# Performance work log

Measured on AMD Instinct MI355X. Metric: run time of the kernel, lower is better.

Reference implementation:

```python
import jax, jax.numpy as jnp
import numpy as np

EPS = 1e-6
N_HEADS = 16
D_NOPE = 128   # qk_nope_head_dim == head_dim
D_ROPE = 64    # qk_rope_head_dim == head_dim // 2


def rmsnorm(x, g):
    # matches torch RMSNorm: normalize in fp32 then scale
    xf = x.astype(jnp.float32)
    n = xf * jax.lax.rsqrt(jnp.mean(xf * xf, axis=-1, keepdims=True) + EPS)
    return n.astype(x.dtype) * g


def rope(x):
    # x: [..., S, D]; rotary-embedding-torch convention: interleaved pairs, theta=10000
    S, D = x.shape[-2], x.shape[-1]
    freqs = 1.0 / (10000.0 ** (jnp.arange(0, D, 2, dtype=jnp.float32) / D))  # [D/2]
    ang = jnp.arange(S, dtype=jnp.float32)[:, None] * freqs                   # [S, D/2]
    ang = jnp.repeat(ang, 2, axis=-1)                                         # [S, D]
    cos, sin = jnp.cos(ang), jnp.sin(ang)
    x2 = x.reshape(*x.shape[:-1], D // 2, 2)
    xr = jnp.stack([-x2[..., 1], x2[..., 0]], axis=-1).reshape(x.shape)
    return x * cos + xr * sin


def setup_inputs() -> dict:
    key = jax.random.key(0)
    ks = jax.random.split(key, 9)
    def w(k, shape):
        return jax.random.normal(k, shape, dtype=jnp.float32) * (shape[0] ** -0.5)
    return {
        "x": jax.random.normal(ks[0], (2, 2048, 2048), dtype=jnp.float32),
        "w_dq": w(ks[1], (2048, 512)),
        "g_q": jnp.ones((512,), dtype=jnp.float32),
        "w_uq": w(ks[2], (512, 3072)),
        "w_dkv": w(ks[3], (2048, 512)),
        "g_kv": jnp.ones((512,), dtype=jnp.float32),
        "w_ukrope": w(ks[4], (2048, 64)),
        "w_uv": w(ks[5], (512, 2048)),
        "w_uknope": w(ks[6], (512, 2048)),
        "w_o": w(ks[7], (2048, 2048)),
    }


def reference(x, w_dq, g_q, w_uq, w_dkv, g_kv, w_ukrope, w_uv, w_uknope, w_o):
    B, S, _ = x.shape
    H, Dn, Dr = N_HEADS, D_NOPE, D_ROPE

    # low-rank KV path
    kv = rmsnorm(x @ w_dkv, g_kv)                                    # [B,S,512]
    k_nope = (kv @ w_uknope).reshape(B, S, H, Dn).transpose(0, 2, 1, 3)  # [B,H,S,Dn]
    v = (kv @ w_uv).reshape(B, S, H, Dn).transpose(0, 2, 1, 3)           # [B,H,S,Dn]
    k_rope = rope(x @ w_ukrope)                                      # [B,S,Dr] shared across heads

    # low-rank Q path
    q = rmsnorm(x @ w_dq, g_q) @ w_uq                                # [B,S,H*(Dn+Dr)]
    q = q.reshape(B, S, H, Dn + Dr).transpose(0, 2, 1, 3)            # [B,H,S,Dn+Dr]
    q_nope, q_rope = q[..., :Dn], rope(q[..., Dn:])

    # causal SDPA with head-shared rope keys folded into scores
    scale = 1.0 / jnp.sqrt(jnp.float32(Dn + Dr))
    scores = jnp.einsum("bhqd,bhkd->bhqk", q_nope, k_nope)
    scores = scores + jnp.einsum("bhqd,bkd->bhqk", q_rope, k_rope)
    scores = scores * scale
    causal = jnp.tril(jnp.ones((S, S), dtype=bool))
    scores = jnp.where(causal, scores, -jnp.inf)
    attn = jax.nn.softmax(scores, axis=-1)
    out = jnp.einsum("bhqk,bhkd->bhqd", attn, v)                     # [B,H,S,Dn]
    out = out.transpose(0, 2, 1, 3).reshape(B, S, H * Dn)
    return out @ w_o
```

## Files before the change

### kernel.cpp

```cpp
#include <hip/hip_runtime.h>
#include <hip/hip_bf16.h>


#define S_ 2048
#define H_ 16

typedef __bf16 bf16_t;
typedef __bf16 bf16x8 __attribute__((ext_vector_type(8)));
typedef __bf16 bf16x4_t __attribute__((ext_vector_type(4)));
typedef float f32x4 __attribute__((ext_vector_type(4)));

#define ASYNC_COPY16(gsrc, ldst)                                              \
  __builtin_amdgcn_global_load_lds(                                           \
      (const __attribute__((address_space(1))) void*)(gsrc),                  \
      (__attribute__((address_space(3))) void*)(ldst), 16, 0, 0)

#define QSCALE 0.1041177003f
#define FIXM 16.0f

struct TWDesc { const float* src; bf16_t* dst; int K, N, boff; };
struct TW7 { TWDesc d[7]; };

__global__ __launch_bounds__(256) void prep_all(const float* __restrict__ x,
                                                bf16_t* __restrict__ xb,
                                                float2* __restrict__ tab,
                                                TW7 t7) {
  __shared__ float t[32][33];
  int bid = blockIdx.x;
  int tid = threadIdx.x;
  if (bid < 8192) {
    int i = bid * 256 + tid;
    float4 v = ((const float4*)x)[i];
    bf16x4_t o = {(bf16_t)v.x, (bf16_t)v.y, (bf16_t)v.z, (bf16_t)v.w};
    ((bf16x4_t*)xb)[i] = o;
  } else if (bid < 8448) {
    int i = (bid - 8192) * 256 + tid;
    int j = i & 31, s = i >> 5;
    float freq = powf(10000.f, -(float)(2 * j) / 64.f);
    float ang = (float)s * freq;
    tab[i] = make_float2(cosf(ang), sinf(ang));
  } else {
    int e = 0;
#pragma unroll
    for (int i = 1; i < 7; i++)
      if (bid >= t7.d[i].boff) e = i;
    const float* src = t7.d[e].src;
    bf16_t* dst = t7.d[e].dst;
    int K = t7.d[e].K, N = t7.d[e].N;
    int lb = bid - t7.d[e].boff;
    int nx = N >> 5;
    int n0 = (lb % nx) * 32, k0 = (lb / nx) * 32;
    int tx = tid & 31, ty = tid >> 5;
#pragma unroll
    for (int i = 0; i < 4; i++)
      t[ty + i * 8][tx] = src[(size_t)(k0 + ty + i * 8) * N + n0 + tx];
    __syncthreads();
#pragma unroll
    for (int i = 0; i < 4; i++)
      dst[(size_t)(n0 + ty + i * 8) * K + k0 + tx] = (bf16_t)t[tx][ty + i * 8];
  }
}

template <typename OT, int MODE>
__global__ __launch_bounds__(256) void gemm_bt(const bf16_t* __restrict__ A,
                                               const bf16_t* __restrict__ Bt,
                                               OT* __restrict__ C, int M, int N,
                                               int K, int lda) {
  __shared__ bf16_t Asm[128 * 32];
  __shared__ bf16_t Bsm[128 * 32];
  int tid = threadIdx.x;
  int w = tid >> 6, lane = tid & 63;
  int lrow = lane & 15, lgrp = lane >> 4;
  int wr = w >> 1, wc = w & 1;
  int bm = blockIdx.y * 128, bn = blockIdx.x * 128;

  const bf16_t* Ab = A + (size_t)bm * lda;
  const bf16_t* Bb = Bt + (size_t)bn * K;

  int srow = (w << 5) + (lane >> 2);
  int schunk = lane & 3;

  int ra[4], rb[4];
#pragma unroll
  for (int m = 0; m < 4; m++) {
    int rowA = wr * 64 + m * 16 + lrow;
    ra[m] = rowA * 64 + ((lgrp * 16) ^ (((rowA >> 1) & 3) << 4));
    int rowB = wc * 64 + m * 16 + lrow;
    rb[m] = rowB * 64 + ((lgrp * 16) ^ (((rowB >> 1) & 3) << 4));
  }

  f32x4 acc[4][4] = {};

  for (int k0 = 0; k0 < K; k0 += 32) {
#pragma unroll
    for (int j = 0; j < 2; j++) {
      int row = srow + j * 16;
      int cs = schunk ^ ((row >> 1) & 3);
      ASYNC_COPY16(Ab + (size_t)row * lda + k0 + cs * 8,
                   (char*)Asm + (w << 11) + (j << 10));
      ASYNC_COPY16(Bb + (size_t)row * K + k0 + cs * 8,
                   (char*)Bsm + (w << 11) + (j << 10));
    }
    __syncthreads();
    bf16x8 af[4], bfr[4];
#pragma unroll
    for (int m = 0; m < 4; m++) {
      af[m] = *(const bf16x8*)((const char*)Asm + ra[m]);
      bfr[m] = *(const bf16x8*)((const char*)Bsm + rb[m]);
    }
#pragma unroll
    for (int m = 0; m < 4; m++)
#pragma unroll
      for (int n = 0; n < 4; n++)
        acc[m][n] =
            __builtin_amdgcn_mfma_f32_16x16x32_bf16(af[m], bfr[n], acc[m][n], 0, 0, 0);
    __syncthreads();
  }

#pragma unroll
  for (int m = 0; m < 4; m++)
#pragma unroll
    for (int n = 0; n < 4; n++)
#pragma unroll
      for (int j = 0; j < 4; j++) {
        int row = bm + wr * 64 + m * 16 + lgrp * 4 + j;
        int col = bn + wc * 64 + n * 16 + lrow;
        float val = acc[m][n][j];
        if (MODE == 0) {
          C[(size_t)row * N + col] = (OT)val;
        } else if (MODE == 6) {
          if (col < 1024) {
            ((bf16_t*)C)[(size_t)row * 1024 + col] = (bf16_t)val;
          } else if (col < 1088) {
            float* krf = (float*)((bf16_t*)C + (size_t)M * 1024);
            krf[(size_t)row * 64 + (col - 1024)] = val;
          }
        }
      }
}

__global__ __launch_bounds__(256) void gemm_qkv(const bf16_t* __restrict__ y,
                                                const bf16_t* __restrict__ uq_t,
                                                const bf16_t* __restrict__ ukn_t,
                                                bf16_t* __restrict__ Qp,
                                                bf16_t* __restrict__ Kp) {
  const int K = 512, lda = 1024, M = 4096;
  __shared__ bf16_t Asm[128 * 32];
  __shared__ bf16_t Bsm[128 * 32];
  int tid = threadIdx.x;
  int w = tid >> 6, lane = tid & 63;
  int lrow = lane & 15, lgrp = lane >> 4;
  int wr = w >> 1, wc = w & 1;
  int bnx = blockIdx.x;
  bool qpath = bnx < 24;
  const bf16_t* A = qpath ? y : (y + 512);
  const bf16_t* Bt = qpath ? uq_t : ukn_t;
  int bm = blockIdx.y * 128;
  int bn = (qpath ? bnx : bnx - 24) * 128;
  (void)M;

  const bf16_t* Ab = A + (size_t)bm * lda;
  const bf16_t* Bb = Bt + (size_t)bn * K;

  int srow = (w << 5) + (lane >> 2);
  int schunk = lane & 3;

  int ra[4], rb[4];
#pragma unroll
  for (int m = 0; m < 4; m++) {
    int rowA = wr * 64 + m * 16 + lrow;
    ra[m] = rowA * 64 + ((lgrp * 16) ^ (((rowA >> 1) & 3) << 4));
    int rowB = wc * 64 + m * 16 + lrow;
    rb[m] = rowB * 64 + ((lgrp * 16) ^ (((rowB >> 1) & 3) << 4));
  }

  f32x4 acc[4][4] = {};

  for (int k0 = 0; k0 < K; k0 += 32) {
#pragma unroll
    for (int j = 0; j < 2; j++) {
      int row = srow + j * 16;
      int cs = schunk ^ ((row >> 1) & 3);
      ASYNC_COPY16(Ab + (size_t)row * lda + k0 + cs * 8,
                   (char*)Asm + (w << 11) + (j << 10));
      ASYNC_COPY16(Bb + (size_t)row * K + k0 + cs * 8,
                   (char*)Bsm + (w << 11) + (j << 10));
    }
    __syncthreads();
    bf16x8 af[4], bfr[4];
#pragma unroll
    for (int m = 0; m < 4; m++) {
      af[m] = *(const bf16x8*)((const char*)Asm + ra[m]);
      bfr[m] = *(const bf16x8*)((const char*)Bsm + rb[m]);
    }
#pragma unroll
    for (int m = 0; m < 4; m++)
#pragma unroll
      for (int n = 0; n < 4; n++)
        acc[m][n] =
            __builtin_amdgcn_mfma_f32_16x16x32_bf16(af[m], bfr[n], acc[m][n], 0, 0, 0);
    __syncthreads();
  }

#pragma unroll
  for (int m = 0; m < 4; m++)
#pragma unroll
    for (int n = 0; n < 4; n++)
#pragma unroll
      for (int j = 0; j < 4; j++) {
        int row = bm + wr * 64 + m * 16 + lgrp * 4 + j;
        int col = bn + wc * 64 + n * 16 + lrow;
        float val = acc[m][n][j];
        int b = row >> 11, s = row & (S_ - 1);
        if (qpath) {
          unsigned h = (unsigned)col / 192u, f = (unsigned)col % 192u;
          Qp[((size_t)((b << 4) + h) * S_ + s) * 192 + f] = (bf16_t)(val * QSCALE);
        } else if (col < 2048) {
          int h = col >> 7, d = col & 127;
          Kp[((size_t)((b << 4) + h) * S_ + s) * 192 + d] = (bf16_t)val;
        } else {
          int c2 = col - 2048;
          int h = c2 >> 7, d = c2 & 127;
          bf16_t* VtP = Kp + (size_t)32 * S_ * 192;
          VtP[((size_t)((b << 4) + h) * 128 + d) * S_ + s] = (bf16_t)val;
        }
      }
}

__global__ __launch_bounds__(256) void rmsnorm_both(bf16_t* __restrict__ y,
                                                    const float* __restrict__ g_q,
                                                    const float* __restrict__ g_kv) {
  int bid = blockIdx.x;
  int row = bid >> 1, seg = bid & 1;
  const float* g = seg ? g_kv : g_q;
  bf16_t* p = y + (size_t)row * 1024 + seg * 512;
  int t = threadIdx.x;
  float v0 = (float)p[t], v1 = (float)p[t + 256];
  __shared__ float red[256];
  red[t] = v0 * v0 + v1 * v1;
  __syncthreads();
  for (int s = 128; s > 0; s >>= 1) {
    if (t < s) red[t] += red[t + s];
    __syncthreads();
  }
  float r = rsqrtf(red[0] / 512.f + 1e-6f);
  p[t] = (bf16_t)(v0 * r * g[t]);
  p[t + 256] = (bf16_t)(v1 * r * g[t + 256]);
}

__global__ __launch_bounds__(256) void rope_both(const float* __restrict__ krf,
                                                 const float2* __restrict__ tab,
                                                 bf16_t* __restrict__ Kp,
                                                 bf16_t* __restrict__ Qp) {
  int i = blockIdx.x * 256 + threadIdx.x;
  if (i < 4096 * 32) {
    int j = i & 31, row = i >> 5;
    int b = row >> 11, s = row & (S_ - 1);
    float v0 = krf[(size_t)row * 64 + 2 * j];
    float v1 = krf[(size_t)row * 64 + 2 * j + 1];
    float2 cs = tab[(s << 5) + j];
    bf16_t r0 = (bf16_t)(v0 * cs.x - v1 * cs.y);
    bf16_t r1 = (bf16_t)(v1 * cs.x + v0 * cs.y);
    union { bf16_t h[2]; unsigned u; } pk;
    pk.h[0] = r0; pk.h[1] = r1;
#pragma unroll
    for (int h = 0; h < 16; h++) {
      size_t base = ((size_t)((b << 4) + h) * S_ + s) * 192 + 128 + 2 * j;
      *(unsigned*)(Kp + base) = pk.u;
    }
  } else {
    int i2 = i - 4096 * 32;
    int j = i2 & 31;
    int s = (i2 >> 5) & (S_ - 1);
    int bh = i2 >> 16;
    float2 cs = tab[(s << 5) + j];
    size_t base = ((size_t)bh * S_ + s) * 192 + 128 + 2 * j;
    float x0 = (float)Qp[base], x1 = (float)Qp[base + 1];
    Qp[base] = (bf16_t)(x0 * cs.x - x1 * cs.y);
    Qp[base + 1] = (bf16_t)(x1 * cs.x + x0 * cs.y);
  }
}

__global__ __launch_bounds__(512) void flash_attn5(
    const bf16_t* __restrict__ Qp,
    const bf16_t* __restrict__ Kp,
    const bf16_t* __restrict__ Vt,
    bf16_t* __restrict__ o) {
  __shared__ alignas(16) char kls[2 * 64 * 384];
  __shared__ alignas(16) char vls[2 * 128 * 128];
  __shared__ alignas(16) bf16_t psh[8][16 * 64];

  int bid = blockIdx.x;
  int rest = bid >> 3;
  int p = rest & 7;
  int bh = (bid & 7) + ((rest >> 3) << 3);
  int b = bh >> 4;

  int tid = threadIdx.x;
  int w = tid >> 6;
  int lane = tid & 63;
  int lrow = lane & 15;
  int lgrp = lane >> 4;
  bf16_t* pw = &psh[w][0];

  const char* Kbh = (const char*)(Kp + (size_t)bh * S_ * 192);
  const char* Vbh = (const char*)(Vt + (size_t)bh * 128 * S_);

  int ksrc[3], vsrc[2];
#pragma unroll
  for (int r = 0; r < 3; r++) {
    int c = tid + r * 512;
    int row = c / 24, pos = c - row * 24;
    ksrc[r] = row * 384 + ((pos ^ (row & 7)) << 4);
  }
#pragma unroll
  for (int r = 0; r < 2; r++) {
    int c = tid + r * 512;
    int d = c >> 3, pos = c & 7;
    vsrc[r] = d * 4096 + ((pos ^ (d & 7)) << 4);
  }

  int kchk[6], vchk[2];
#pragma unroll
  for (int ks = 0; ks < 6; ks++)
    kchk[ks] = (((lgrp + ks * 4) ^ (lrow & 7)) << 4) + lrow * 384;
#pragma unroll
  for (int ks = 0; ks < 2; ks++)
    vchk[ks] = (((lgrp + ks * 4) ^ (lrow & 7)) << 4) + lrow * 128;

#pragma unroll 1
  for (int half = 0; half < 2; half++) {
    const int qt = half ? p : (15 - p);
    const int qb = qt * 128 + w * 16;
    const bf16_t* Qb = Qp + ((size_t)bh * S_ + qb) * 192;

    bf16x8 qf[6];
#pragma unroll
    for (int ks = 0; ks < 6; ks++)
      qf[ks] = *(const bf16x8*)(Qb + (size_t)lrow * 192 + ks * 32 + lgrp * 8);

    f32x4 acc[8];
#pragma unroll
    for (int i = 0; i < 8; i++) acc[i] = f32x4{0.f, 0.f, 0.f, 0.f};
    float lsum[4] = {0.f, 0.f, 0.f, 0.f};

    const int nk = 2 * qt + 2;
    {
      const char* kb = Kbh;
#pragma unroll
      for (int r = 0; r < 3; r++)
        ASYNC_COPY16(kb + ksrc[r], kls + (tid + r * 512) * 16);
#pragma unroll
      for (int r = 0; r < 2; r++)
        ASYNC_COPY16(Vbh + vsrc[r], vls + (tid + r * 512) * 16);
    }
    __syncthreads();

    int cur = 0;
#pragma unroll 1
    for (int kt = 0; kt < nk; kt++) {
      if (kt + 1 < nk) {
        const char* kb = Kbh + (size_t)(kt + 1) * (64 * 384);
        char* kd = kls + (cur ^ 1) * 24576;
#pragma unroll
        for (int r = 0; r < 3; r++)
          ASYNC_COPY16(kb + ksrc[r], kd + (tid + r * 512) * 16);
        const char* vb2 = Vbh + (size_t)(kt + 1) * 128;
        char* vd = vls + (cur ^ 1) * 16384;
#pragma unroll
        for (int r = 0; r < 2; r++)
          ASYNC_COPY16(vb2 + vsrc[r], vd + (tid + r * 512) * 16);
      }

      const char* kbuf = kls + cur * 24576;
      f32x4 sc[4];
#pragma unroll
      for (int cb = 0; cb < 4; cb++) {
        f32x4 s = f32x4{0.f, 0.f, 0.f, 0.f};
        const char* kp = kbuf + cb * 6144;
#pragma unroll
        for (int ks = 0; ks < 6; ks++) {
          bf16x8 kf = *(const bf16x8*)(kp + kchk[ks]);
          s = __builtin_amdgcn_mfma_f32_16x16x32_bf16(qf[ks], kf, s, 0, 0, 0);
        }
        sc[cb] = s;
      }
      if (kt >= 2 * qt) {
#pragma unroll
        for (int cb = 0; cb < 4; cb++)
#pragma unroll
          for (int r = 0; r < 4; r++) {
            int col = kt * 64 + cb * 16 + lrow;
            int row = qb + lgrp * 4 + r;
            if (col > row) sc[cb][r] = -1e30f;
          }
      }
#pragma unroll
      for (int r = 0; r < 4; r++) {
        float ps = 0.f;
#pragma unroll
        for (int cb = 0; cb < 4; cb++) {
          float e = exp2f(sc[cb][r] - FIXM);
          sc[cb][r] = e;
          ps += e;
        }
        lsum[r] += ps;
      }
#pragma unroll
      for (int r = 0; r < 4; r++) {
        int row = lgrp * 4 + r;
#pragma unroll
        for (int cb = 0; cb < 4; cb++) {
          int byte = (row * 128 + (cb * 16 + lrow) * 2) ^ ((row & 7) << 4);
          *(bf16_t*)((char*)pw + byte) = (bf16_t)sc[cb][r];
        }
      }
      bf16x8 pa[2];
#pragma unroll
      for (int ks = 0; ks < 2; ks++) {
        int byte = (lrow * 128 + ks * 64 + lgrp * 16) ^ ((lrow & 7) << 4);
        pa[ks] = *(const bf16x8*)((char*)pw + byte);
      }
      const char* vbuf = vls + cur * 16384;
#pragma unroll
      for (int cbv = 0; cbv < 8; cbv++) {
        const char* vp = vbuf + cbv * 2048;
        f32x4 a = acc[cbv];
#pragma unroll
        for (int ks = 0; ks < 2; ks++) {
          bf16x8 vf = *(const bf16x8*)(vp + vchk[ks]);
          a = __builtin_amdgcn_mfma_f32_16x16x32_bf16(pa[ks], vf, a, 0, 0, 0);
        }
        acc[cbv] = a;
      }
      __syncthreads();
      cur ^= 1;
    }
#pragma unroll
    for (int r = 0; r < 4; r++) {
      float s = lsum[r];
      s += __shfl_xor(s, 1);
      s += __shfl_xor(s, 2);
      s += __shfl_xor(s, 4);
      s += __shfl_xor(s, 8);
      float inv = 1.f / s;
      int row = qb + lgrp * 4 + r;
      bf16_t* op = o + (size_t)(b * S_ + row) * 2048 + (bh & 15) * 128;
#pragma unroll
      for (int cbv = 0; cbv < 8; cbv++)
        op[cbv * 16 + lrow] = (bf16_t)(acc[cbv][r] * inv);
    }
  }
}

extern "C" void kernel_launch(void* const* d_in, const int* in_sizes, int n_in,
                              void* d_out, int out_size, void* d_ws, size_t ws_size,
                              hipStream_t stream) {
  const float* x        = (const float*)d_in[0];
  const float* w_dq     = (const float*)d_in[1];
  const float* g_q      = (const float*)d_in[2];
  const float* w_uq     = (const float*)d_in[3];
  const float* w_dkv    = (const float*)d_in[4];
  const float* g_kv     = (const float*)d_in[5];
  const float* w_ukrope = (const float*)d_in[6];
  const float* w_uv     = (const float*)d_in[7];
  const float* w_uknope = (const float*)d_in[8];
  const float* w_o      = (const float*)d_in[9];
  float* out = (float*)d_out;

  const int M = 4096;
  bf16_t* wb = (bf16_t*)d_ws;
  size_t off = 0;
  bf16_t* xb   = wb + off; off += (size_t)M * 2048;
  bf16_t* y    = wb + off; off += (size_t)M * 1024;
  float*  krf  = (float*)(wb + off); off += (size_t)M * 128;
  bf16_t* dq_t = wb + off; off += (size_t)512 * 2048;
  bf16_t* dkv_t= wb + off; off += (size_t)512 * 2048;
  bf16_t* ukr_t= wb + off; off += (size_t)128 * 2048;
  bf16_t* uq_t = wb + off; off += (size_t)3072 * 512;
  bf16_t* ukn_t= wb + off; off += (size_t)2048 * 512;
  bf16_t* uv_t = wb + off; off += (size_t)2048 * 512;
  bf16_t* o_t  = wb + off; off += (size_t)2048 * 2048;
  bf16_t* Qp   = wb + off; off += (size_t)32 * S_ * 192;
  bf16_t* Kp   = wb + off; off += (size_t)32 * S_ * 192;
  bf16_t* Vt   = wb + off; off += (size_t)32 * 128 * S_;
  float2* tab  = (float2*)(wb + off); off += (size_t)S_ * 32 * 4;
  bf16_t* ao = xb;
  (void)dkv_t; (void)ukr_t; (void)uv_t;

  dim3 blk(256);
  TW7 t7;
  t7.d[0] = {w_dq,     dq_t,  2048, 512,  8448};
  t7.d[1] = {w_dkv,    dkv_t, 2048, 512,  9472};
  t7.d[2] = {w_ukrope, ukr_t, 2048, 64,   10496};
  t7.d[3] = {w_uq,     uq_t,  512,  3072, 10624};
  t7.d[4] = {w_uknope, ukn_t, 512,  2048, 12160};
  t7.d[5] = {w_uv,     uv_t,  512,  2048, 13184};
  t7.d[6] = {w_o,      o_t,   2048, 2048, 14208};
  prep_all<<<18304, blk, 0, stream>>>(x, xb, tab, t7);
  gemm_bt<bf16_t, 6><<<dim3(9, 32), blk, 0, stream>>>(xb, dq_t, y, M, 1152, 2048,
                                                      2048);
  rmsnorm_both<<<8192, blk, 0, stream>>>(y, g_q, g_kv);
  gemm_qkv<<<dim3(56, 32), blk, 0, stream>>>(y, uq_t, ukn_t, Qp, Kp);
  rope_both<<<8704, blk, 0, stream>>>(krf, tab, Kp, Qp);
  flash_attn5<<<256, dim3(512), 0, stream>>>(Qp, Kp, Vt, ao);
  gemm_bt<float, 0><<<dim3(16, 32), blk, 0, stream>>>(ao, o_t, out, M, 2048, 2048,
                                                      2048);
}
```

Measured before the change: 287.2 us.

## Double-buffer LDS tiles in the GEMM kernels to prefetch the next K-slice

Both the generic gemm_bt and the fused gemm_qkv kernel now use two LDS buffers for the A and B tiles. The async global-to-LDS copy for the next K-step is issued before the current tile is read and fed to MFMA, so the load latency can overlap with compute. The barrier at the end of each iteration is meant to ensure the prefetch has landed before the buffers swap. This doubles LDS use per block, which may lower occupancy, and it only touches the projection GEMMs, not the attention kernel.

```diff
diff --git a/kernel.cpp b/kernel.cpp
--- a/kernel.cpp
+++ b/kernel.cpp
@@ -66,8 +66,8 @@
                                                const bf16_t* __restrict__ Bt,
                                                OT* __restrict__ C, int M, int N,
                                                int K, int lda) {
-  __shared__ bf16_t Asm[128 * 32];
-  __shared__ bf16_t Bsm[128 * 32];
+  __shared__ bf16_t Asm[2][128 * 32];
+  __shared__ bf16_t Bsm[2][128 * 32];
   int tid = threadIdx.x;
   int w = tid >> 6, lane = tid & 63;
   int lrow = lane & 15, lgrp = lane >> 4;
@@ -91,22 +91,30 @@
 
   f32x4 acc[4][4] = {};
 
-  for (int k0 = 0; k0 < K; k0 += 32) {
+  auto stage = [&](int k0, int bufi) {
 #pragma unroll
     for (int j = 0; j < 2; j++) {
       int row = srow + j * 16;
       int cs = schunk ^ ((row >> 1) & 3);
       ASYNC_COPY16(Ab + (size_t)row * lda + k0 + cs * 8,
-                   (char*)Asm + (w << 11) + (j << 10));
+                   (char*)Asm[bufi] + (w << 11) + (j << 10));
       ASYNC_COPY16(Bb + (size_t)row * K + k0 + cs * 8,
-                   (char*)Bsm + (w << 11) + (j << 10));
-    }
-    __syncthreads();
+                   (char*)Bsm[bufi] + (w << 11) + (j << 10));
+    }
+  };
+
+  const int niter = K >> 5;
+  stage(0, 0);
+  __syncthreads();
+  int cur = 0;
+#pragma unroll 1
+  for (int kt = 0; kt < niter; kt++) {
+    if (kt + 1 < niter) stage((kt + 1) << 5, cur ^ 1);
     bf16x8 af[4], bfr[4];
 #pragma unroll
     for (int m = 0; m < 4; m++) {
-      af[m] = *(const bf16x8*)((const char*)Asm + ra[m]);
-      bfr[m] = *(const bf16x8*)((const char*)Bsm + rb[m]);
+      af[m] = *(const bf16x8*)((const char*)Asm[cur] + ra[m]);
+      bfr[m] = *(const bf16x8*)((const char*)Bsm[cur] + rb[m]);
     }
 #pragma unroll
     for (int m = 0; m < 4; m++)
@@ -115,6 +123,7 @@
         acc[m][n] =
             __builtin_amdgcn_mfma_f32_16x16x32_bf16(af[m], bfr[n], acc[m][n], 0, 0, 0);
     __syncthreads();
+    cur ^= 1;
   }
 
 #pragma unroll
@@ -144,9 +153,9 @@
                                                 const bf16_t* __restrict__ ukn_t,
                                                 bf16_t* __restrict__ Qp,
                                                 bf16_t* __restrict__ Kp) {
-  const int K = 512, lda = 1024, M = 4096;
-  __shared__ bf16_t Asm[128 * 32];
-  __shared__ bf16_t Bsm[128 * 32];
+  const int K = 512, lda = 1024;
+  __shared__ bf16_t Asm[2][128 * 32];
+  __shared__ bf16_t Bsm[2][128 * 32];
   int tid = threadIdx.x;
   int w = tid >> 6, lane = tid & 63;
   int lrow = lane & 15, lgrp = lane >> 4;
@@ -157,7 +166,6 @@
   const bf16_t* Bt = qpath ? uq_t : ukn_t;
   int bm = blockIdx.y * 128;
   int bn = (qpath ? bnx : bnx - 24) * 128;
-  (void)M;
 
   const bf16_t* Ab = A + (size_t)bm * lda;
   const bf16_t* Bb = Bt + (size_t)bn * K;
@@ -176,22 +184,30 @@
 
   f32x4 acc[4][4] = {};
 
-  for (int k0 = 0; k0 < K; k0 += 32) {
+  auto stage = [&](int k0, int bufi) {
 #pragma unroll
     for (int j = 0; j < 2; j++) {
       int row = srow + j * 16;
       int cs = schunk ^ ((row >> 1) & 3);
       ASYNC_COPY16(Ab + (size_t)row * lda + k0 + cs * 8,
-                   (char*)Asm + (w << 11) + (j << 10));
+                   (char*)Asm[bufi] + (w << 11) + (j << 10));
       ASYNC_COPY16(Bb + (size_t)row * K + k0 + cs * 8,
-                   (char*)Bsm + (w << 11) + (j << 10));
-    }
-    __syncthreads();
+                   (char*)Bsm[bufi] + (w << 11) + (j << 10));
+    }
+  };
+
+  const int niter = K >> 5;
+  stage(0, 0);
+  __syncthreads();
+  int cur = 0;
+#pragma unroll 1
+  for (int kt = 0; kt < niter; kt++) {
+    if (kt + 1 < niter) stage((kt + 1) << 5, cur ^ 1);
     bf16x8 af[4], bfr[4];
 #pragma unroll
     for (int m = 0; m < 4; m++) {
-      af[m] = *(const bf16x8*)((const char*)Asm + ra[m]);
-      bfr[m] = *(const bf16x8*)((const char*)Bsm + rb[m]);
+      af[m] = *(const bf16x8*)((const char*)Asm[cur] + ra[m]);
+      bfr[m] = *(const bf16x8*)((const char*)Bsm[cur] + rb[m]);
     }
 #pragma unroll
     for (int m = 0; m < 4; m++)
@@ -200,6 +216,7 @@
         acc[m][n] =
             __builtin_amdgcn_mfma_f32_16x16x32_bf16(af[m], bfr[n], acc[m][n], 0, 0, 0);
     __syncthreads();
+    cur ^= 1;
   }
 
 #pragma unroll
```

New measurement: 273.4 us. -4.8%, faster.
